# Kernel tuning notes

Hardware: AMD Instinct MI355X
Metric: run time of the kernel (lower is better)

## Reference

```python
import jax, jax.numpy as jnp
import numpy as np

B, N_PER, F_IN, HID, DEG = 64, 1024, 64, 128, 16
N = B * N_PER
E = N * DEG

def _ceil_k(k):
    return -((-4 * k) // 5)  # ceil(0.8 * k), static python int

def setup_inputs():
    key = jax.random.key(0)
    ks = jax.random.split(key, 16)
    x = jax.random.normal(ks[0], (N, F_IN), jnp.float32)
    # edges are intra-graph: local endpoints in [0, N_PER) offset by graph id
    loc = jax.random.randint(ks[1], (2, E), 0, N_PER, jnp.int32)
    gid = jnp.repeat(jnp.arange(B, dtype=jnp.int32), E // B)
    edge_index = loc + gid[None, :] * N_PER
    batch = jnp.repeat(jnp.arange(B, dtype=jnp.int32), N_PER)
    def lin(k, fi, fo):
        s = 1.0 / float(np.sqrt(fi))
        return jax.random.uniform(k, (fi, fo), jnp.float32, -s, s)
    inp = dict(x=x, edge_index=edge_index, batch=batch)
    inp["Wr1"] = lin(ks[2], F_IN, HID); inp["Wn1"] = lin(ks[3], F_IN, HID); inp["b1"] = jnp.zeros((HID,), jnp.float32)
    inp["Wr2"] = lin(ks[4], HID, HID); inp["Wn2"] = lin(ks[5], HID, HID); inp["b2"] = jnp.zeros((HID,), jnp.float32)
    inp["Wr3"] = lin(ks[6], HID, HID); inp["Wn3"] = lin(ks[7], HID, HID); inp["b3"] = jnp.zeros((HID,), jnp.float32)
    inp["p1"] = jax.random.normal(ks[8], (HID,), jnp.float32)
    inp["p2"] = jax.random.normal(ks[9], (HID,), jnp.float32)
    inp["p3"] = jax.random.normal(ks[10], (HID,), jnp.float32)
    inp["l1w"] = lin(ks[11], 2 * HID, HID); inp["l1b"] = jnp.zeros((HID,), jnp.float32)
    inp["l2w"] = lin(ks[12], HID, 2); inp["l2b"] = jnp.zeros((2,), jnp.float32)
    return inp

def _graph_conv(x, src, dst, emask, Wr, Wn, b, n_nodes):
    # x'_i = W1 x_i + sum_{j->i} W2 x_j + b ; masked edges contribute 0
    msg = x[src] * emask[:, None]                                  # [E, H]
    agg = jax.ops.segment_sum(msg, dst, num_segments=n_nodes)     # [N, H]
    return x @ Wr + agg @ Wn + b

def _topk_pool(x, src, dst, emask, p, k_prev):
    # PyG TopKPooling: score = x.p/||p||, keep ceil(0.8*n) per graph,
    # x_out = x[perm] * tanh(score[perm]); relabel+filter edges
    k_new = _ceil_k(k_prev)
    s = (x @ p) / jnp.linalg.norm(p)                               # [B*k_prev]
    vals, idx = jax.lax.top_k(s.reshape(B, k_prev), k_new)        # [B, k_new]
    perm = (idx + jnp.arange(B, dtype=idx.dtype)[:, None] * k_prev).reshape(-1)
    x_new = x[perm] * jnp.tanh(vals.reshape(-1))[:, None]
    inv = jnp.full((B * k_prev,), -1, jnp.int32).at[perm].set(jnp.arange(B * k_new, dtype=jnp.int32))
    ns, nd = inv[src], inv[dst]
    valid = emask * ((ns >= 0) & (nd >= 0)).astype(x.dtype)
    return x_new, jnp.maximum(ns, 0), jnp.maximum(nd, 0), valid, k_new

def _readout(x, k):
    b = jnp.repeat(jnp.arange(B, dtype=jnp.int32), k)
    gmax = jax.ops.segment_max(x, b, num_segments=B)
    gmean = jax.ops.segment_sum(x, b, num_segments=B) / k
    return jnp.concatenate([gmax, gmean], axis=1)                  # [B, 2H]

def reference(x, edge_index, batch, Wr1, Wn1, b1, Wr2, Wn2, b2, Wr3, Wn3, b3, p1, p2, p3, l1w, l1b, l2w, l2b):
    src, dst = edge_index[0], edge_index[1]
    emask = jnp.ones((E,), x.dtype)
    k = N_PER
    convs = [(Wr1, Wn1, b1), (Wr2, Wn2, b2), (Wr3, Wn3, b3)]
    pools = [p1, p2, p3]
    xs = []
    for (Wr, Wn, bb), p in zip(convs, pools):
        x = jax.nn.relu(_graph_conv(x, src, dst, emask, Wr, Wn, bb, B * k))
        x, src, dst, emask, k = _topk_pool(x, src, dst, emask, p, k)
        xs.append(_readout(x, k))
    h = xs[0] + xs[1] + xs[2]
    h = jax.nn.relu(h @ l1w + l1b)
    # F.dropout(p=0.5) skipped: eval-mode reference
    h = jax.nn.relu(h @ l2w + l2b)
    return jax.nn.log_softmax(h, axis=-1)
```

## Files before the change

kernel.cpp:

```cpp
#include <hip/hip_runtime.h>
#include <hip/hip_bf16.h>
#include <math.h>

#define NN   65536
#define NPER 1024
#define NE   1048576
#define NB   64

typedef __attribute__((ext_vector_type(8))) short short8;
typedef __attribute__((ext_vector_type(4))) float f32x4;


__global__ __launch_bounds__(256) void count_kernel(const int* __restrict__ ei, int* __restrict__ cnt){
  int e = blockIdx.x*256 + threadIdx.x;
  if (e < NE) atomicAdd(&cnt[ei[NE + e]], 1);
}

__global__ __launch_bounds__(1024) void scan1_kernel(const int* __restrict__ cnt,
      int* __restrict__ loc, int* __restrict__ bsum){
  __shared__ int wsum[16];
  int t = threadIdx.x;
  int i = blockIdx.x*1024 + t;
  int lane = t & 63, wid = t >> 6;
  int v = cnt[i];
  int s = v;
  #pragma unroll
  for (int d = 1; d < 64; d <<= 1){
    int src = (lane >= d) ? (lane - d) : lane;
    int u = __shfl(s, src);
    if (lane >= d) s += u;
  }
  if (lane == 63) wsum[wid] = s;
  __syncthreads();
  if (wid == 0){
    int ws = (lane < 16) ? wsum[lane] : 0;
    #pragma unroll
    for (int d = 1; d < 16; d <<= 1){
      int src = (lane >= d) ? (lane - d) : lane;
      int u = __shfl(ws, src);
      if (lane >= d) ws += u;
    }
    if (lane < 16) wsum[lane] = ws;
  }
  __syncthreads();
  int base = (wid > 0) ? wsum[wid - 1] : 0;
  loc[i] = base + s - v;
  if (t == 1023) bsum[blockIdx.x] = base + s;
}

__global__ __launch_bounds__(64) void scan2_kernel(const int* __restrict__ bsum, int* __restrict__ boff){
  int t = threadIdx.x;
  int v = bsum[t];
  int s = v;
  #pragma unroll
  for (int d = 1; d < 64; d <<= 1){
    int src = (t >= d) ? (t - d) : t;
    int u = __shfl(s, src);
    if (t >= d) s += u;
  }
  boff[t] = s - v;
}

__global__ __launch_bounds__(1024) void scan3_kernel(const int* __restrict__ loc, const int* __restrict__ boff,
      int* __restrict__ off, int* __restrict__ cursor){
  int i = blockIdx.x*1024 + threadIdx.x;
  int v = loc[i] + boff[blockIdx.x];
  off[i] = v;
  cursor[i] = v;
  if (i == NN - 1) off[NN] = NE;
}

__global__ __launch_bounds__(256) void fill_kernel(const int* __restrict__ ei, int* cursor, int* __restrict__ adj){
  int e = blockIdx.x*256 + threadIdx.x;
  if (e < NE){
    int pos = atomicAdd(&cursor[ei[NE + e]], 1);
    adj[pos] = ei[e];
  }
}


__global__ __launch_bounds__(256) void gather_kernel(const float* __restrict__ x, int stride, int F,
      const int* __restrict__ off, const int* __restrict__ adj, float* __restrict__ agg,
      const int* __restrict__ alive, const float* __restrict__ scale){
  int bid = blockIdx.x;
  bid = (bid & 7) * (gridDim.x >> 3) + (bid >> 3);
  int w = (bid*256 + (int)threadIdx.x) >> 6;
  int lane = threadIdx.x & 63;
  if (w >= NN) return;
  if (alive && !alive[w]) return;
  int s0 = off[w], s1 = off[w+1];
  if (F == 64){
    int sub = lane >> 4;
    int fl  = (lane & 15) * 4;
    float4 a[4];
    #pragma unroll
    for (int i = 0; i < 4; ++i) a[i] = make_float4(0.f,0.f,0.f,0.f);
    for (int e = s0; e < s1; e += 16){
      int ss[4]; float tv[4];
      #pragma unroll
      for (int i = 0; i < 4; ++i){
        int ei = e + 4*i + sub;
        bool okE = ei < s1;
        ss[i] = adj[okE ? ei : (s1 - 1)];
        tv[i] = okE ? 1.f : 0.f;
      }
      #pragma unroll
      for (int i = 0; i < 4; ++i){
        float4 v = *(const float4*)&x[(size_t)ss[i]*stride + fl];
        a[i].x = fmaf(v.x, tv[i], a[i].x);
        a[i].y = fmaf(v.y, tv[i], a[i].y);
        a[i].z = fmaf(v.z, tv[i], a[i].z);
        a[i].w = fmaf(v.w, tv[i], a[i].w);
      }
    }
    float4 r;
    r.x = (a[0].x + a[1].x) + (a[2].x + a[3].x);
    r.y = (a[0].y + a[1].y) + (a[2].y + a[3].y);
    r.z = (a[0].z + a[1].z) + (a[2].z + a[3].z);
    r.w = (a[0].w + a[1].w) + (a[2].w + a[3].w);
    #pragma unroll
    for (int m = 16; m <= 32; m <<= 1){
      r.x += __shfl_xor(r.x, m);
      r.y += __shfl_xor(r.y, m);
      r.z += __shfl_xor(r.z, m);
      r.w += __shfl_xor(r.w, m);
    }
    if (lane < 16) *(float4*)&agg[(size_t)w*128 + fl] = r;
  } else {
    int sub = lane >> 5;
    int fl  = (lane & 31) * 4;
    float4 a[8];
    #pragma unroll
    for (int i = 0; i < 8; ++i) a[i] = make_float4(0.f,0.f,0.f,0.f);
    for (int e = s0; e < s1; e += 16){
      int ss[8]; float tv[8];
      #pragma unroll
      for (int i = 0; i < 8; ++i){
        int ei = e + 2*i + sub;
        bool okE = ei < s1;
        int s = adj[okE ? ei : (s1 - 1)];
        ss[i] = s;
        float t = scale[s];
        tv[i] = okE ? t : 0.f;
      }
      #pragma unroll
      for (int i = 0; i < 8; ++i){
        float4 v = *(const float4*)&x[(size_t)ss[i]*stride + fl];
        a[i].x = fmaf(v.x, tv[i], a[i].x);
        a[i].y = fmaf(v.y, tv[i], a[i].y);
        a[i].z = fmaf(v.z, tv[i], a[i].z);
        a[i].w = fmaf(v.w, tv[i], a[i].w);
      }
    }
    float4 r;
    r.x = (a[0].x+a[1].x)+(a[2].x+a[3].x)+((a[4].x+a[5].x)+(a[6].x+a[7].x));
    r.y = (a[0].y+a[1].y)+(a[2].y+a[3].y)+((a[4].y+a[5].y)+(a[6].y+a[7].y));
    r.z = (a[0].z+a[1].z)+(a[2].z+a[3].z)+((a[4].z+a[5].z)+(a[6].z+a[7].z));
    r.w = (a[0].w+a[1].w)+(a[2].w+a[3].w)+((a[4].w+a[5].w)+(a[6].w+a[7].w));
    r.x += __shfl_xor(r.x, 32);
    r.y += __shfl_xor(r.y, 32);
    r.z += __shfl_xor(r.z, 32);
    r.w += __shfl_xor(r.w, 32);
    if (lane < 32) *(float4*)&agg[(size_t)w*128 + fl] = r;
  }
}


__global__ __launch_bounds__(256) void wsplit_kernel(const float* __restrict__ Wr, const float* __restrict__ Wn,
      int Kx, int Kcat, unsigned short* __restrict__ WTh, unsigned short* __restrict__ WTl){
  int idx = blockIdx.x*256 + threadIdx.x;
  if (idx >= Kcat*128) return;
  int c = idx & 127, k = idx >> 7;
  float w = (k < Kx) ? Wr[k*128 + c] : Wn[(k - Kx)*128 + c];
  __hip_bfloat16 h = __float2bfloat16(w);
  float hf = __bfloat162float(h);
  __hip_bfloat16 l = __float2bfloat16(w - hf);
  WTh[(size_t)c*Kcat + k] = reinterpret_cast<unsigned short&>(h);
  WTl[(size_t)c*Kcat + k] = reinterpret_cast<unsigned short&>(l);
}


__global__ __launch_bounds__(256, 2) void conv_kernel(const float* __restrict__ xsrc, int strideX, int ntx,
      const float* aggb, int nta,
      const unsigned short* __restrict__ WTh, const unsigned short* __restrict__ WTl, int Kcat,
      const float* __restrict__ bias, const float* __restrict__ p, const float* __restrict__ scaleX,
      float* yout, float* __restrict__ score){
  __shared__ unsigned short XhL[128*32], XlL[128*32];
  __shared__ unsigned short WhL[128*32], WlL[128*32];
  __shared__ float sbuf[128*2];
  const int tid = threadIdx.x;
  const int row0 = blockIdx.x * 128;
  const int srow = tid & 127;
  const int shalf = tid >> 7;
  const int lane = tid & 63;
  const int wid = tid >> 6;
  const int wr = wid >> 1, wc = wid & 1;
  const int l15 = lane & 15, lkq = lane >> 4;

  const float xscale = scaleX ? scaleX[row0 + srow] : 1.f;

  f32x4 acc[4][4];
  #pragma unroll
  for (int m = 0; m < 4; ++m)
    #pragma unroll
    for (int j = 0; j < 4; ++j)
      acc[m][j] = (f32x4){0.f, 0.f, 0.f, 0.f};

  const int nt = ntx + nta;
  for (int t = 0; t < nt; ++t){
    __syncthreads();
    {
      const float* Xs   = (t < ntx) ? xsrc : aggb;
      const int stride  = (t < ntx) ? strideX : 128;
      const int kc      = (t < ntx) ? t*32 : (t - ntx)*32;
      const float sc    = (t < ntx) ? xscale : 1.f;
      #pragma unroll
      for (int kq2 = 0; kq2 < 2; ++kq2){
        const int kq = shalf*2 + kq2;
        const float* xp = Xs + (size_t)(row0 + srow)*stride + kc + kq*8;
        float4 v0 = *(const float4*)(xp);
        float4 v1 = *(const float4*)(xp + 4);
        float vv[8] = {v0.x*sc, v0.y*sc, v0.z*sc, v0.w*sc,
                       v1.x*sc, v1.y*sc, v1.z*sc, v1.w*sc};
        short8 hs, ls;
        #pragma unroll
        for (int q = 0; q < 8; ++q){
          __hip_bfloat16 h = __float2bfloat16(vv[q]);
          float hf = __bfloat162float(h);
          __hip_bfloat16 lo = __float2bfloat16(vv[q] - hf);
          hs[q] = reinterpret_cast<short&>(h);
          ls[q] = reinterpret_cast<short&>(lo);
        }
        const int kqph = kq ^ (srow & 3);
        *(short8*)&XhL[srow*32 + kqph*8] = hs;
        *(short8*)&XlL[srow*32 + kqph*8] = ls;
      }
      const int kcw = t*32;
      #pragma unroll
      for (int kq2 = 0; kq2 < 2; ++kq2){
        const int kq = shalf*2 + kq2;
        short8 h = *(const short8*)&WTh[(size_t)srow*Kcat + kcw + kq*8];
        short8 l = *(const short8*)&WTl[(size_t)srow*Kcat + kcw + kq*8];
        const int kqph = kq ^ (srow & 3);
        *(short8*)&WhL[srow*32 + kqph*8] = h;
        *(short8*)&WlL[srow*32 + kqph*8] = l;
      }
    }
    __syncthreads();
    short8 bh[4], bl[4];
    #pragma unroll
    for (int j = 0; j < 4; ++j){
      const int col = wc*64 + j*16 + l15;
      const int offb = col*32 + (lkq ^ (col & 3))*8;
      bh[j] = *(const short8*)&WhL[offb];
      bl[j] = *(const short8*)&WlL[offb];
    }
    #pragma unroll
    for (int m = 0; m < 4; ++m){
      const int row = wr*64 + m*16 + l15;
      const int offa = row*32 + (lkq ^ (row & 3))*8;
      short8 ah = *(const short8*)&XhL[offa];
      short8 al = *(const short8*)&XlL[offa];
      #pragma unroll
      for (int j = 0; j < 4; ++j){
        acc[m][j] = __builtin_amdgcn_mfma_f32_16x16x32_bf16(ah, bh[j], acc[m][j], 0, 0, 0);
        acc[m][j] = __builtin_amdgcn_mfma_f32_16x16x32_bf16(ah, bl[j], acc[m][j], 0, 0, 0);
        acc[m][j] = __builtin_amdgcn_mfma_f32_16x16x32_bf16(al, bh[j], acc[m][j], 0, 0, 0);
      }
    }
  }

  #pragma unroll
  for (int m = 0; m < 4; ++m){
    float prt[4] = {0.f, 0.f, 0.f, 0.f};
    #pragma unroll
    for (int j = 0; j < 4; ++j){
      const int col = wc*64 + j*16 + l15;
      const float bcol = bias[col];
      const float pcol = p[col];
      f32x4 a = acc[m][j];
      #pragma unroll
      for (int r = 0; r < 4; ++r){
        const int row = wr*64 + m*16 + lkq*4 + r;
        float y = fmaxf(a[r] + bcol, 0.f);
        yout[(size_t)(row0 + row)*128 + col] = y;
        prt[r] = fmaf(y, pcol, prt[r]);
      }
    }
    #pragma unroll
    for (int r = 0; r < 4; ++r){
      #pragma unroll
      for (int msk = 8; msk >= 1; msk >>= 1) prt[r] += __shfl_xor(prt[r], msk);
      if (l15 == 0) sbuf[(wr*64 + m*16 + lkq*4 + r)*2 + wc] = prt[r];
    }
  }
  __syncthreads();
  if (tid < 128) score[row0 + tid] = sbuf[tid*2] + sbuf[tid*2 + 1];
}


__global__ __launch_bounds__(1024) void topk_kernel(const float* __restrict__ score, const int* __restrict__ alive_cur,
      int* __restrict__ alive_next, float* __restrict__ scale, const float* __restrict__ p, int m){
  __shared__ float lv[1024];
  __shared__ int   li[1024];
  __shared__ float rnorm;
  const int g = blockIdx.x, t = threadIdx.x;
  if (t < 64){
    float v0 = p[t], v1 = p[t + 64];
    float ss = v0*v0 + v1*v1;
    #pragma unroll
    for (int mm = 32; mm >= 1; mm >>= 1) ss += __shfl_xor(ss, mm);
    if (t == 0) rnorm = rsqrtf(ss);
  }
  const int node = g*NPER + t;
  bool ok = alive_cur ? (alive_cur[node] != 0) : true;
  float v = ok ? score[node] : -INFINITY;
  int idx = node;
  alive_next[node] = 0;
  scale[node] = 0.f;

  auto cex_shfl = [&](int stride, bool dirUp){
    float vj = __shfl_xor(v, stride);
    int   ij = __shfl_xor(idx, stride);
    bool iAmLow = (t & stride) == 0;
    bool mineFirst = (v > vj) || (v == vj && idx < ij);
    bool takeMine = ((dirUp == iAmLow) == mineFirst);
    v   = takeMine ? v   : vj;
    idx = takeMine ? idx : ij;
  };
  auto cex_lds = [&](int stride, bool dirUp){
    __syncthreads();
    lv[t] = v; li[t] = idx;
    __syncthreads();
    float vj = lv[t ^ stride];
    int   ij = li[t ^ stride];
    bool iAmLow = (t & stride) == 0;
    bool mineFirst = (v > vj) || (v == vj && idx < ij);
    bool takeMine = ((dirUp == iAmLow) == mineFirst);
    v   = takeMine ? v   : vj;
    idx = takeMine ? idx : ij;
  };

  #pragma unroll
  for (int size = 2; size <= 64; size <<= 1){
    const bool dirUp = (t & size) == 0;
    for (int stride = size >> 1; stride >= 1; stride >>= 1)
      cex_shfl(stride, dirUp);
  }
  #pragma unroll
  for (int size = 128; size <= 1024; size <<= 1){
    const bool dirUp = (t & size) == 0;
    for (int stride = size >> 1; stride >= 64; stride >>= 1)
      cex_lds(stride, dirUp);
    for (int stride = 32; stride >= 1; stride >>= 1)
      cex_shfl(stride, dirUp);
  }

  if (t < m){
    alive_next[idx] = 1;
    scale[idx] = tanhf(v * rnorm);
  }
}


__global__ __launch_bounds__(1024) void readout_kernel(const float* __restrict__ y,
      const int* __restrict__ alive, const float* __restrict__ scale,
      float* __restrict__ h, int m){
  __shared__ float smx[32][33];
  __shared__ float ssm[32][33];
  int g = blockIdx.x;
  int fq = blockIdx.y;
  int t = threadIdx.x;
  int c  = t >> 5;
  int lf = t & 31;
  int f  = fq*32 + lf;
  int base = g*NPER;
  float mx = -INFINITY, sm = 0.f;
  #pragma unroll 4
  for (int i = 0; i < 32; ++i){
    int node = base + c + i*32;
    int al = alive[node];
    float v = y[(size_t)node*128 + f];
    float o = v * scale[node];
    mx = al ? fmaxf(mx, o) : mx;
    sm += o;
  }
  smx[c][lf] = mx; ssm[c][lf] = sm;
  __syncthreads();
  for (int s = 16; s > 0; s >>= 1){
    if (c < s){
      smx[c][lf] = fmaxf(smx[c][lf], smx[c+s][lf]);
      ssm[c][lf] += ssm[c+s][lf];
    }
    __syncthreads();
  }
  if (c == 0){
    h[g*256 + f]       += smx[0][lf];
    h[g*256 + 128 + f] += ssm[0][lf] / (float)m;
  }
}


__global__ __launch_bounds__(128) void final_kernel(const float* __restrict__ h,
      const float* __restrict__ l1w, const float* __restrict__ l1b,
      const float* __restrict__ l2w, const float* __restrict__ l2b,
      float* __restrict__ out){
  int g = blockIdx.x, t = threadIdx.x;
  __shared__ float hrow[256];
  __shared__ float red0[128], red1[128];
  hrow[t]       = h[g*256 + t];
  hrow[t + 128] = h[g*256 + 128 + t];
  __syncthreads();
  float a = l1b[t];
  for (int k = 0; k < 256; ++k) a = fmaf(hrow[k], l1w[k*128 + t], a);
  a = fmaxf(a, 0.f);
  red0[t] = a * l2w[t*2 + 0];
  red1[t] = a * l2w[t*2 + 1];
  __syncthreads();
  for (int s = 64; s > 0; s >>= 1){
    if (t < s){ red0[t] += red0[t + s]; red1[t] += red1[t + s]; }
    __syncthreads();
  }
  if (t == 0){
    float z0 = fmaxf(red0[0] + l2b[0], 0.f);
    float z1 = fmaxf(red1[0] + l2b[1], 0.f);
    float mz = fmaxf(z0, z1);
    float lse = mz + logf(expf(z0 - mz) + expf(z1 - mz));
    out[g*2 + 0] = z0 - lse;
    out[g*2 + 1] = z1 - lse;
  }
}


static inline size_t alignup(size_t x){ return (x + 255) & ~(size_t)255; }

extern "C" void kernel_launch(void* const* d_in, const int* in_sizes, int n_in,
                              void* d_out, int out_size, void* d_ws, size_t ws_size,
                              hipStream_t stream) {
  const float* x_in = (const float*)d_in[0];
  const int*   ei   = (const int*)d_in[1];
  const float* Wr[3] = {(const float*)d_in[3], (const float*)d_in[6], (const float*)d_in[9]};
  const float* Wn[3] = {(const float*)d_in[4], (const float*)d_in[7], (const float*)d_in[10]};
  const float* bs[3] = {(const float*)d_in[5], (const float*)d_in[8], (const float*)d_in[11]};
  const float* ps[3] = {(const float*)d_in[12], (const float*)d_in[13], (const float*)d_in[14]};
  const float* l1w = (const float*)d_in[15];
  const float* l1b = (const float*)d_in[16];
  const float* l2w = (const float*)d_in[17];
  const float* l2b = (const float*)d_in[18];
  float* out = (float*)d_out;

  char* w = (char*)d_ws;
  size_t o = 0;
  auto take = [&](size_t bytes) -> void* { void* p = w + o; o = alignup(o + bytes); return p; };
  int*   off    = (int*)  take((size_t)(NN + 1) * 4);
  int*   adj    = (int*)  take((size_t)NE * 4);
  int*   cnt    = (int*)  take((size_t)NN * 4);
  int*   loc    = (int*)  take((size_t)NN * 4);
  int*   cursor = (int*)  take((size_t)NN * 4);
  int*   bsum   = (int*)  take(64 * 4);
  int*   boff   = (int*)  take(64 * 4);
  int*   aliveA = (int*)  take((size_t)NN * 4);
  int*   aliveB = (int*)  take((size_t)NN * 4);
  float* scale  = (float*)take((size_t)NN * 4);
  float* score  = (float*)take((size_t)NN * 4);
  float* h      = (float*)take((size_t)NB * 256 * 4);
  unsigned short* WTh = (unsigned short*)take((size_t)128 * 256 * 2);
  unsigned short* WTl = (unsigned short*)take((size_t)128 * 256 * 2);
  float* A      = (float*)take((size_t)NN * 128 * 4);
  float* Bb     = (float*)take((size_t)NN * 128 * 4);
  (void)ws_size; (void)n_in; (void)in_sizes; (void)out_size;

  hipMemsetAsync(cnt, 0, (size_t)NN * 4, stream);
  count_kernel<<<NE/256, 256, 0, stream>>>(ei, cnt);
  scan1_kernel<<<NN/1024, 1024, 0, stream>>>(cnt, loc, bsum);
  scan2_kernel<<<1, 64, 0, stream>>>(bsum, boff);
  scan3_kernel<<<NN/1024, 1024, 0, stream>>>(loc, boff, off, cursor);
  fill_kernel<<<NE/256, 256, 0, stream>>>(ei, cursor, adj);
  hipMemsetAsync(h, 0, (size_t)NB * 256 * 4, stream);

  const int MS[3] = {820, 656, 525};
  int* aliveCur = nullptr;
  int* aliveNext = aliveA;
  float* bufs[2] = {Bb, A};
  for (int l = 0; l < 3; ++l){
    const int Kx = (l == 0) ? 64 : 128;
    const int Ka = (l == 0) ? 64 : 128;
    const int Kcat = Kx + Ka;
    float* aggb = bufs[l & 1];
    wsplit_kernel<<<(Kcat*128 + 255)/256, 256, 0, stream>>>(Wr[l], Wn[l], Kx, Kcat, WTh, WTl);
    if (l == 0){
      gather_kernel<<<NN*64/256, 256, 0, stream>>>(x_in, 64, 64, off, adj, aggb, nullptr, nullptr);
      conv_kernel<<<NN/128, 256, 0, stream>>>(x_in, 64, Kx/32, aggb, Ka/32, WTh, WTl, Kcat,
                                              bs[0], ps[0], nullptr, aggb, score);
    } else {
      const float* ysrc = bufs[(l - 1) & 1];
      gather_kernel<<<NN*64/256, 256, 0, stream>>>(ysrc, 128, 128, off, adj, aggb, aliveCur, scale);
      conv_kernel<<<NN/128, 256, 0, stream>>>(ysrc, 128, Kx/32, aggb, Ka/32, WTh, WTl, Kcat,
                                              bs[l], ps[l], scale, aggb, score);
    }
    topk_kernel<<<NB, 1024, 0, stream>>>(score, aliveCur, aliveNext, scale, ps[l], MS[l]);
    readout_kernel<<<dim3(NB, 4), 1024, 0, stream>>>(aggb, aliveNext, scale, h, MS[l]);
    aliveCur = aliveNext;
    aliveNext = (l == 0) ? aliveB : aliveA;
  }
  final_kernel<<<NB, 128, 0, stream>>>(h, l1w, l1b, l2w, l2b, out);
}
```

Baseline: 327.4 us.

## Compact alive edges before gather and rebalance gather and readout parallelism

Adds a compact_kernel that, for layers 2 and 3, uses a wave ballot to drop neighbours whose scale is zero and writes packed adjacency, per-edge scale and degree arrays. The gather then walks only the surviving edges with a contiguous per-edge scale, so it no longer does random scale lookups or loads for pruned nodes. The gather loops are also restructured to use fewer accumulators and a smaller edge stride. Readout is split into 16-feature slices with four independent accumulators, doubling its grid. This adds an extra kernel launch and extra edge-array traffic in exchange for less wasted gather work.

```diff
diff --git a/kernel.cpp b/kernel.cpp
--- a/kernel.cpp
+++ b/kernel.cpp
@@ -79,38 +79,94 @@
 }
 
 
+__global__ __launch_bounds__(256) void compact_kernel(const int* __restrict__ off, const int* __restrict__ adj,
+      const float* __restrict__ scale, const int* __restrict__ alive,
+      int* __restrict__ adj2, float* __restrict__ scl2, int* __restrict__ deg2){
+  int w = (blockIdx.x*256 + (int)threadIdx.x) >> 6;
+  int lane = threadIdx.x & 63;
+  if (w >= NN) return;
+  if (!alive[w]){ if (lane == 0) deg2[w] = 0; return; }
+  int s0 = off[w], s1 = off[w+1];
+  int base = s0;
+  for (int e0 = s0; e0 < s1; e0 += 64){
+    int e = e0 + lane;
+    bool okE = e < s1;
+    int s = adj[okE ? e : (s1 - 1)];
+    float t = scale[s];
+    bool keep = okE && (t != 0.f);
+    unsigned long long m = __ballot(keep);
+    int pos = base + __popcll(m & ((1ull << lane) - 1ull));
+    if (keep){ adj2[pos] = s; scl2[pos] = t; }
+    base += __popcll(m);
+  }
+  if (lane == 0) deg2[w] = base - s0;
+}
+
+
 __global__ __launch_bounds__(256) void gather_kernel(const float* __restrict__ x, int stride, int F,
-      const int* __restrict__ off, const int* __restrict__ adj, float* __restrict__ agg,
-      const int* __restrict__ alive, const float* __restrict__ scale){
+      const int* __restrict__ off, const int* __restrict__ adj, const float* __restrict__ scl,
+      const int* __restrict__ deg2, float* __restrict__ agg, const int* __restrict__ alive){
   int bid = blockIdx.x;
   bid = (bid & 7) * (gridDim.x >> 3) + (bid >> 3);
   int w = (bid*256 + (int)threadIdx.x) >> 6;
   int lane = threadIdx.x & 63;
   if (w >= NN) return;
   if (alive && !alive[w]) return;
-  int s0 = off[w], s1 = off[w+1];
+  int s0 = off[w];
+  int s1 = deg2 ? (s0 + deg2[w]) : off[w+1];
   if (F == 64){
     int sub = lane >> 4;
     int fl  = (lane & 15) * 4;
+    float4 a0 = make_float4(0.f,0.f,0.f,0.f), a1 = a0;
+    if (s1 > s0){
+      for (int e = s0; e < s1; e += 8){
+        int e0 = e + sub, e1 = e + 4 + sub;
+        bool ok0 = e0 < s1, ok1 = e1 < s1;
+        int sA = adj[ok0 ? e0 : (s1 - 1)];
+        int sB = adj[ok1 ? e1 : (s1 - 1)];
+        float t0 = ok0 ? 1.f : 0.f, t1 = ok1 ? 1.f : 0.f;
+        float4 vA = *(const float4*)&x[(size_t)sA*stride + fl];
+        float4 vB = *(const float4*)&x[(size_t)sB*stride + fl];
+        a0.x = fmaf(vA.x, t0, a0.x); a0.y = fmaf(vA.y, t0, a0.y);
+        a0.z = fmaf(vA.z, t0, a0.z); a0.w = fmaf(vA.w, t0, a0.w);
+        a1.x = fmaf(vB.x, t1, a1.x); a1.y = fmaf(vB.y, t1, a1.y);
+        a1.z = fmaf(vB.z, t1, a1.z); a1.w = fmaf(vB.w, t1, a1.w);
+      }
+    }
+    a0.x += a1.x; a0.y += a1.y; a0.z += a1.z; a0.w += a1.w;
+    #pragma unroll
+    for (int m = 16; m <= 32; m <<= 1){
+      a0.x += __shfl_xor(a0.x, m);
+      a0.y += __shfl_xor(a0.y, m);
+      a0.z += __shfl_xor(a0.z, m);
+      a0.w += __shfl_xor(a0.w, m);
+    }
+    if (lane < 16) *(float4*)&agg[(size_t)w*128 + fl] = a0;
+  } else {
+    int sub = lane >> 5;
+    int fl  = (lane & 31) * 4;
     float4 a[4];
     #pragma unroll
     for (int i = 0; i < 4; ++i) a[i] = make_float4(0.f,0.f,0.f,0.f);
-    for (int e = s0; e < s1; e += 16){
-      int ss[4]; float tv[4];
-      #pragma unroll
-      for (int i = 0; i < 4; ++i){
-        int ei = e + 4*i + sub;
-        bool okE = ei < s1;
-        ss[i] = adj[okE ? ei : (s1 - 1)];
-        tv[i] = okE ? 1.f : 0.f;
-      }
-      #pragma unroll
-      for (int i = 0; i < 4; ++i){
-        float4 v = *(const float4*)&x[(size_t)ss[i]*stride + fl];
-        a[i].x = fmaf(v.x, tv[i], a[i].x);
-        a[i].y = fmaf(v.y, tv[i], a[i].y);
-        a[i].z = fmaf(v.z, tv[i], a[i].z);
-        a[i].w = fmaf(v.w, tv[i], a[i].w);
+    if (s1 > s0){
+      for (int e = s0; e < s1; e += 8){
+        int ss[4]; float tv[4];
+        #pragma unroll
+        for (int i = 0; i < 4; ++i){
+          int ei = e + 2*i + sub;
+          bool okE = ei < s1;
+          int ii = okE ? ei : (s1 - 1);
+          ss[i] = adj[ii];
+          tv[i] = okE ? scl[ii] : 0.f;
+        }
+        #pragma unroll
+        for (int i = 0; i < 4; ++i){
+          float4 v = *(const float4*)&x[(size_t)ss[i]*stride + fl];
+          a[i].x = fmaf(v.x, tv[i], a[i].x);
+          a[i].y = fmaf(v.y, tv[i], a[i].y);
+          a[i].z = fmaf(v.z, tv[i], a[i].z);
+          a[i].w = fmaf(v.w, tv[i], a[i].w);
+        }
       }
     }
     float4 r;
@@ -118,45 +174,6 @@
     r.y = (a[0].y + a[1].y) + (a[2].y + a[3].y);
     r.z = (a[0].z + a[1].z) + (a[2].z + a[3].z);
     r.w = (a[0].w + a[1].w) + (a[2].w + a[3].w);
-    #pragma unroll
-    for (int m = 16; m <= 32; m <<= 1){
-      r.x += __shfl_xor(r.x, m);
-      r.y += __shfl_xor(r.y, m);
-      r.z += __shfl_xor(r.z, m);
-      r.w += __shfl_xor(r.w, m);
-    }
-    if (lane < 16) *(float4*)&agg[(size_t)w*128 + fl] = r;
-  } else {
-    int sub = lane >> 5;
-    int fl  = (lane & 31) * 4;
-    float4 a[8];
-    #pragma unroll
-    for (int i = 0; i < 8; ++i) a[i] = make_float4(0.f,0.f,0.f,0.f);
-    for (int e = s0; e < s1; e += 16){
-      int ss[8]; float tv[8];
-      #pragma unroll
-      for (int i = 0; i < 8; ++i){
-        int ei = e + 2*i + sub;
-        bool okE = ei < s1;
-        int s = adj[okE ? ei : (s1 - 1)];
-        ss[i] = s;
-        float t = scale[s];
-        tv[i] = okE ? t : 0.f;
-      }
-      #pragma unroll
-      for (int i = 0; i < 8; ++i){
-        float4 v = *(const float4*)&x[(size_t)ss[i]*stride + fl];
-        a[i].x = fmaf(v.x, tv[i], a[i].x);
-        a[i].y = fmaf(v.y, tv[i], a[i].y);
-        a[i].z = fmaf(v.z, tv[i], a[i].z);
-        a[i].w = fmaf(v.w, tv[i], a[i].w);
-      }
-    }
-    float4 r;
-    r.x = (a[0].x+a[1].x)+(a[2].x+a[3].x)+((a[4].x+a[5].x)+(a[6].x+a[7].x));
-    r.y = (a[0].y+a[1].y)+(a[2].y+a[3].y)+((a[4].y+a[5].y)+(a[6].y+a[7].y));
-    r.z = (a[0].z+a[1].z)+(a[2].z+a[3].z)+((a[4].z+a[5].z)+(a[6].z+a[7].z));
-    r.w = (a[0].w+a[1].w)+(a[2].w+a[3].w)+((a[4].w+a[5].w)+(a[6].w+a[7].w));
     r.x += __shfl_xor(r.x, 32);
     r.y += __shfl_xor(r.y, 32);
     r.z += __shfl_xor(r.z, 32);
@@ -366,28 +383,33 @@
 __global__ __launch_bounds__(1024) void readout_kernel(const float* __restrict__ y,
       const int* __restrict__ alive, const float* __restrict__ scale,
       float* __restrict__ h, int m){
-  __shared__ float smx[32][33];
-  __shared__ float ssm[32][33];
+  __shared__ float smx[64][17];
+  __shared__ float ssm[64][17];
   int g = blockIdx.x;
   int fq = blockIdx.y;
   int t = threadIdx.x;
-  int c  = t >> 5;
-  int lf = t & 31;
-  int f  = fq*32 + lf;
+  int c  = t >> 4;
+  int lf = t & 15;
+  int f  = fq*16 + lf;
   int base = g*NPER;
-  float mx = -INFINITY, sm = 0.f;
-  #pragma unroll 4
-  for (int i = 0; i < 32; ++i){
-    int node = base + c + i*32;
-    int al = alive[node];
-    float v = y[(size_t)node*128 + f];
-    float o = v * scale[node];
-    mx = al ? fmaxf(mx, o) : mx;
-    sm += o;
-  }
-  smx[c][lf] = mx; ssm[c][lf] = sm;
+  float mx[4] = {-INFINITY, -INFINITY, -INFINITY, -INFINITY};
+  float sm[4] = {0.f, 0.f, 0.f, 0.f};
+  #pragma unroll
+  for (int i = 0; i < 16; i += 4){
+    #pragma unroll
+    for (int q = 0; q < 4; ++q){
+      int node = base + c + (i + q)*64;
+      int al = alive[node];
+      float o = y[(size_t)node*128 + f] * scale[node];
+      mx[q] = al ? fmaxf(mx[q], o) : mx[q];
+      sm[q] += o;
+    }
+  }
+  float mxa = fmaxf(fmaxf(mx[0], mx[1]), fmaxf(mx[2], mx[3]));
+  float sma = (sm[0] + sm[1]) + (sm[2] + sm[3]);
+  smx[c][lf] = mxa; ssm[c][lf] = sma;
   __syncthreads();
-  for (int s = 16; s > 0; s >>= 1){
+  for (int s = 32; s > 0; s >>= 1){
     if (c < s){
       smx[c][lf] = fmaxf(smx[c][lf], smx[c+s][lf]);
       ssm[c][lf] += ssm[c+s][lf];
@@ -454,6 +476,9 @@
   auto take = [&](size_t bytes) -> void* { void* p = w + o; o = alignup(o + bytes); return p; };
   int*   off    = (int*)  take((size_t)(NN + 1) * 4);
   int*   adj    = (int*)  take((size_t)NE * 4);
+  int*   adj2   = (int*)  take((size_t)NE * 4);
+  float* scl2   = (float*)take((size_t)NE * 4);
+  int*   deg2   = (int*)  take((size_t)NN * 4);
   int*   cnt    = (int*)  take((size_t)NN * 4);
   int*   loc    = (int*)  take((size_t)NN * 4);
   int*   cursor = (int*)  take((size_t)NN * 4);
@@ -489,17 +514,18 @@
     float* aggb = bufs[l & 1];
     wsplit_kernel<<<(Kcat*128 + 255)/256, 256, 0, stream>>>(Wr[l], Wn[l], Kx, Kcat, WTh, WTl);
     if (l == 0){
-      gather_kernel<<<NN*64/256, 256, 0, stream>>>(x_in, 64, 64, off, adj, aggb, nullptr, nullptr);
+      gather_kernel<<<NN*64/256, 256, 0, stream>>>(x_in, 64, 64, off, adj, nullptr, nullptr, aggb, nullptr);
       conv_kernel<<<NN/128, 256, 0, stream>>>(x_in, 64, Kx/32, aggb, Ka/32, WTh, WTl, Kcat,
                                               bs[0], ps[0], nullptr, aggb, score);
     } else {
       const float* ysrc = bufs[(l - 1) & 1];
-      gather_kernel<<<NN*64/256, 256, 0, stream>>>(ysrc, 128, 128, off, adj, aggb, aliveCur, scale);
+      compact_kernel<<<NN*64/256, 256, 0, stream>>>(off, adj, scale, aliveCur, adj2, scl2, deg2);
+      gather_kernel<<<NN*64/256, 256, 0, stream>>>(ysrc, 128, 128, off, adj2, scl2, deg2, aggb, aliveCur);
       conv_kernel<<<NN/128, 256, 0, stream>>>(ysrc, 128, Kx/32, aggb, Ka/32, WTh, WTl, Kcat,
                                               bs[l], ps[l], scale, aggb, score);
     }
     topk_kernel<<<NB, 1024, 0, stream>>>(score, aliveCur, aliveNext, scale, ps[l], MS[l]);
-    readout_kernel<<<dim3(NB, 4), 1024, 0, stream>>>(aggb, aliveNext, scale, h, MS[l]);
+    readout_kernel<<<dim3(NB, 8), 1024, 0, stream>>>(aggb, aliveNext, scale, h, MS[l]);
     aliveCur = aliveNext;
     aliveNext = (l == 0) ? aliveB : aliveA;
   }
```

Result: faster. 317.0 us (-3.2%).
